# Optimization experiments

Hardware: AMD Instinct MI355X
Metric: run time of the kernel (lower is better)

The kernel has to match this reference:

```python
import jax, jax.numpy as jnp
import numpy as np

B, H, S = 2048, 1024, 128


def setup_inputs() -> dict:
    key = jax.random.key(0)
    ks = jax.random.split(key, 8)
    s = 0.05  # keep gates out of saturation, roughly 1/sqrt(H) init scale
    return {
        "hidden": jax.random.normal(ks[0], (1, B, H), jnp.float32) * s,
        "cell": jax.random.normal(ks[1], (1, B, H), jnp.float32) * s,
        "W_ih": jax.random.normal(ks[2], (4 * H, 1), jnp.float32) * s,
        "W_hh": jax.random.normal(ks[3], (4 * H, H), jnp.float32) * s,
        "b_ih": jax.random.normal(ks[4], (4 * H,), jnp.float32) * s,
        "b_hh": jax.random.normal(ks[5], (4 * H,), jnp.float32) * s,
        "W_fc": jax.random.normal(ks[6], (S, H), jnp.float32) * s,
        "b_fc": jax.random.normal(ks[7], (S,), jnp.float32) * s,
    }


def reference(hidden, cell, W_ih, W_hh, b_ih, b_hh, W_fc, b_fc):
    # prediction from per-step head fc_i fed back as next input.
    h0 = hidden[0]  # [B, H] (num_layers = 1)
    c0 = cell[0]
    b = b_ih + b_hh  # [4H]
    x0 = jnp.zeros((h0.shape[0], 1), h0.dtype)  # initial zero input [B, 1]

    def step(carry, fc_t):
        h, c, x = carry
        Wt, bt = fc_t  # Wt: [H], bt: scalar
        gates = x @ W_ih.T + h @ W_hh.T + b  # [B, 4H], torch gate order i,f,g,o
        i, f, g, o = jnp.split(gates, 4, axis=-1)
        c = jax.nn.sigmoid(f) * c + jax.nn.sigmoid(i) * jnp.tanh(g)
        h = jax.nn.sigmoid(o) * jnp.tanh(c)
        pred = h @ Wt + bt  # [B] (Linear(H,1) then squeeze)
        return (h, c, pred[:, None]), pred

    _, preds = jax.lax.scan(step, (h0, c0, x0), (W_fc, b_fc))  # preds: [S, B]
    return preds.T  # [B, S]
```

## Files before the change

kernel.cpp:

```cpp
#include <hip/hip_runtime.h>
#include <hip/hip_bf16.h>
#include <stdint.h>

#define B_SZ 2048
#define H_SZ 1024
#define S_SZ 128
#define G4   4096
#define BK   64
#define NKK  16
#define BM   128
#define BN   256
#define NJT  16
#define NBLK 256

typedef short short8 __attribute__((ext_vector_type(8)));
typedef int   intx4  __attribute__((ext_vector_type(4)));
typedef float floatx4 __attribute__((ext_vector_type(4)));

#define AS1 __attribute__((address_space(1)))
#define AS3 __attribute__((address_space(3)))

__device__ ushort g_Wp[G4 * H_SZ];
__device__ ushort g_h[2][B_SZ * H_SZ];
__device__ float  g_wih[G4];
__device__ float  g_bias[G4];
__device__ float  g_pp[2][B_SZ][NJT];
__device__ unsigned g_leaf[8 * 32];
__device__ unsigned g_root;
__device__ unsigned g_gen;

__device__ __forceinline__ ushort f2bf(float f) {
  unsigned u = __float_as_uint(f);
  return (ushort)((u + 0x7FFFu + ((u >> 16) & 1u)) >> 16);
}
__device__ __forceinline__ float fsig(float x) { return 1.f / (1.f + __expf(-x)); }
__device__ __forceinline__ float ftanh(float x) { return 1.f - 2.f / (__expf(2.f * x) + 1.f); }

__device__ __forceinline__ void gload16(const void* g, void* l) {
  __builtin_amdgcn_global_load_lds((const AS1 void*)g, (AS3 void*)l, 16, 0, 0);
}

__device__ __forceinline__ void grid_barrier(int grp) {
  __syncthreads();
  if (threadIdx.x == 0) {
    __builtin_amdgcn_fence(__ATOMIC_RELEASE, "agent");
    unsigned gen = __hip_atomic_load(&g_gen, __ATOMIC_RELAXED, __HIP_MEMORY_SCOPE_AGENT);
    unsigned a = __hip_atomic_fetch_add(&g_leaf[grp * 32], 1u, __ATOMIC_RELAXED,
                                        __HIP_MEMORY_SCOPE_AGENT);
    if (a == 31u) {
      __hip_atomic_store(&g_leaf[grp * 32], 0u, __ATOMIC_RELAXED, __HIP_MEMORY_SCOPE_AGENT);
      unsigned r = __hip_atomic_fetch_add(&g_root, 1u, __ATOMIC_RELAXED,
                                          __HIP_MEMORY_SCOPE_AGENT);
      if (r == 7u) {
        __hip_atomic_store(&g_root, 0u, __ATOMIC_RELAXED, __HIP_MEMORY_SCOPE_AGENT);
        __hip_atomic_store(&g_gen, gen + 1u, __ATOMIC_RELAXED, __HIP_MEMORY_SCOPE_AGENT);
      } else {
        while (__hip_atomic_load(&g_gen, __ATOMIC_RELAXED, __HIP_MEMORY_SCOPE_AGENT) == gen)
          __builtin_amdgcn_s_sleep(2);
      }
    } else {
      while (__hip_atomic_load(&g_gen, __ATOMIC_RELAXED, __HIP_MEMORY_SCOPE_AGENT) == gen)
        __builtin_amdgcn_s_sleep(2);
    }
    asm volatile("" ::: "memory");
  }
  __syncthreads();
}


__global__ __launch_bounds__(256) void prep_wpack(const float* __restrict__ Whh) {
  const int gid = blockIdx.x * 256 + threadIdx.x;
  const int j   = gid >> 7;
  const int k8  = (gid & 127) << 3;
  const int gate = (j >> 4) & 3;
  const int h    = ((j >> 6) << 4) | (j & 15);
  const float* src = Whh + (size_t)(gate * H_SZ + h) * H_SZ + k8;
  floatx4 a = *(const floatx4*)src;
  floatx4 b = *(const floatx4*)(src + 4);
  short8 o;
#pragma unroll
  for (int i = 0; i < 4; ++i) o[i] = (short)f2bf(a[i]);
#pragma unroll
  for (int i = 0; i < 4; ++i) o[4 + i] = (short)f2bf(b[i]);
  const size_t dst = (size_t)(j >> 8) * 262144 + (size_t)(k8 >> 6) * 16384 +
                     (size_t)((k8 >> 3) & 7) * 2048 + (size_t)(j & 255) * 8;
  *(short8*)&g_Wp[dst] = o;
}

__global__ __launch_bounds__(256) void prep_misc(const float* __restrict__ Wih,
                                                 const float* __restrict__ bih,
                                                 const float* __restrict__ bhh) {
  if (blockIdx.x == 0) {
    if (threadIdx.x == 0) { g_root = 0u; g_gen = 0u; }
    if (threadIdx.x < 8) g_leaf[threadIdx.x * 32] = 0u;
  }
  const int j = blockIdx.x * 256 + threadIdx.x;
  const int gate = (j >> 4) & 3;
  const int h    = ((j >> 6) << 4) | (j & 15);
  const int jp   = gate * H_SZ + h;
  g_wih[j]  = Wih[jp];
  g_bias[j] = bih[jp] + bhh[jp];
}

__global__ __launch_bounds__(256) void prep_h(const float* __restrict__ hidden) {
  const int gid = blockIdx.x * 256 + threadIdx.x;
  const int o8  = gid << 3;
  short8 o;
#pragma unroll
  for (int i = 0; i < 8; ++i) o[i] = (short)f2bf(hidden[o8 + i]);
  *(short8*)&g_h[0][o8] = o;
}

__global__ __launch_bounds__(512, 1)
void lstm_persistent(const float* __restrict__ cell,
                     const float* __restrict__ Wfc,
                     const float* __restrict__ bfc,
                     float* __restrict__ out) {
  __shared__ ushort Al[2][8256];
  __shared__ ushort Bl[3][16384];
  __shared__ float  xbuf[BM];
  __shared__ float  predp[4 * BM];

  const int tid  = threadIdx.x;
  const int lane = tid & 63;
  const int wid  = tid >> 6;
  const int bid  = blockIdx.x;
  const int grp  = bid & 7;
  const int idx  = bid >> 3;
  const int jt   = (grp << 1) | (idx & 1);
  const int bt   = idx >> 1;
  const int brow = bt * BM;
  const int wr = wid >> 2, wc = wid & 3;
  const int lr = lane & 15, lk = lane >> 4;

  const size_t wbase = (size_t)jt * 262144;
  const size_t abase = (size_t)(brow + (tid >> 2)) * H_SZ + (size_t)(tid & 3) * 16;
  ushort* const awp = &Al[0][((tid & 3) * 2) * 1032 + (tid >> 2) * 8];

  const int hcol = ((jt << 2) + wc) * 16 + lr;
  float wih[4], bb[4];
#pragma unroll
  for (int n = 0; n < 4; ++n) {
    const int col = jt * BN + wc * 64 + n * 16 + lr;
    wih[n] = g_wih[col];
    bb[n]  = g_bias[col];
  }

  float creg[4][4];
#pragma unroll
  for (int m = 0; m < 4; ++m)
#pragma unroll
    for (int r = 0; r < 4; ++r) {
      const int row_l = wr * 64 + m * 16 + lk * 4 + r;
      creg[m][r] = cell[(size_t)(brow + row_l) * H_SZ + hcol];
    }

  intx4 a0, a1, a2, a3;

#define ISSUE_B(I)                                                          \
  {                                                                         \
    const ushort* bs = g_Wp + wbase + (size_t)(I) * 16384 + (size_t)tid * 8;\
    ushort* bd = &Bl[(I) % 3][(tid & 448) * 8];                             \
    gload16(bs, bd);                                                        \
    gload16(bs + 4096, bd + 4096);                                          \
    gload16(bs + 8192, bd + 8192);                                          \
    gload16(bs + 12288, bd + 12288);                                        \
  }

#define ISSUE_A(I, AW0, AW1)                                                \
  {                                                                         \
    const ushort* as_ = hin + abase + (size_t)(I) * 64;                     \
    asm volatile("global_load_dwordx4 %0, %1, off sc0 sc1"                  \
                 : "=v"(AW0) : "v"(as_));                                   \
    asm volatile("global_load_dwordx4 %0, %1, off sc0 sc1"                  \
                 : "=v"(AW1) : "v"(as_ + 8));                               \
  }

#define COMPUTE(BA, BB)                                                     \
  {                                                                         \
    _Pragma("unroll") for (int k2 = 0; k2 < 2; ++k2) {                      \
      const int co = k2 * 4 + lk;                                           \
      short8 a[4], b[4];                                                    \
      _Pragma("unroll") for (int m = 0; m < 4; ++m)                         \
          a[m] = *(const short8*)&Al[BA][co * 1032 + (wr * 64 + m * 16 + lr) * 8]; \
      _Pragma("unroll") for (int n = 0; n < 4; ++n)                         \
          b[n] = *(const short8*)&Bl[BB][co * 2048 + (wc * 64 + n * 16 + lr) * 8]; \
      __builtin_amdgcn_s_setprio(1);                                        \
      _Pragma("unroll") for (int m = 0; m < 4; ++m)                         \
          _Pragma("unroll") for (int n = 0; n < 4; ++n)                     \
              acc[m][n] = __builtin_amdgcn_mfma_f32_16x16x32_bf16(          \
                  a[m], b[n], acc[m][n], 0, 0, 0);                          \
      __builtin_amdgcn_s_setprio(0);                                        \
    }                                                                       \
  }

#define PH(I, AW0, AW1, AR0, AR1)                                           \
  {                                                                         \
    ISSUE_B((I) + 1);                                                       \
    ISSUE_A((I) + 1, AW0, AW1);                                             \
    asm volatile("s_waitcnt vmcnt(6)" ::: "memory");                        \
    __builtin_amdgcn_sched_barrier(0);                                      \
    *(intx4*)(awp + ((I) & 1) * 8256) = AR0;                                \
    *(intx4*)(awp + ((I) & 1) * 8256 + 1032) = AR1;                         \
    asm volatile("s_waitcnt lgkmcnt(0)" ::: "memory");                      \
    __builtin_amdgcn_s_barrier();                                           \
    __builtin_amdgcn_sched_barrier(0);                                      \
    COMPUTE((I) & 1, (I) % 3);                                              \
  }

#define PHLAST                                                              \
  {                                                                         \
    asm volatile("s_waitcnt vmcnt(0)" ::: "memory");                        \
    __builtin_amdgcn_sched_barrier(0);                                      \
    *(intx4*)(awp + 8256) = a2;                                             \
    *(intx4*)(awp + 8256 + 1032) = a3;                                      \
    asm volatile("s_waitcnt lgkmcnt(0)" ::: "memory");                      \
    __builtin_amdgcn_s_barrier();                                           \
    __builtin_amdgcn_sched_barrier(0);                                      \
    COMPUTE(1, 0);                                                          \
  }

  for (int t = 0; t < S_SZ; ++t) {
    const int p = t & 1;
    const ushort* __restrict__ hin = g_h[p];
    ushort* __restrict__ hout      = g_h[p ^ 1];

    floatx4 acc[4][4];
#pragma unroll
    for (int m = 0; m < 4; ++m)
#pragma unroll
      for (int n = 0; n < 4; ++n) acc[m][n] = {0.f, 0.f, 0.f, 0.f};

    ISSUE_B(0);
    ISSUE_A(0, a0, a1);

    PH(0,  a2, a3, a0, a1);
    PH(1,  a0, a1, a2, a3);
    PH(2,  a2, a3, a0, a1);
    PH(3,  a0, a1, a2, a3);
    PH(4,  a2, a3, a0, a1);
    PH(5,  a0, a1, a2, a3);
    PH(6,  a2, a3, a0, a1);
    PH(7,  a0, a1, a2, a3);
    PH(8,  a2, a3, a0, a1);
    PH(9,  a0, a1, a2, a3);
    PH(10, a2, a3, a0, a1);
    PH(11, a0, a1, a2, a3);
    PH(12, a2, a3, a0, a1);
    PH(13, a0, a1, a2, a3);
    PH(14, a2, a3, a0, a1);
    PHLAST;

    if (t > 0 && tid < BM) {
      float s = bfc[t - 1];
      const float* pr = &g_pp[(t - 1) & 1][brow + tid][0];
#pragma unroll
      for (int j = 0; j < NJT; ++j)
        s += __hip_atomic_load(pr + j, __ATOMIC_RELAXED, __HIP_MEMORY_SCOPE_AGENT);
      xbuf[tid] = s;
      if (jt == 0) out[(size_t)(brow + tid) * S_SZ + (t - 1)] = s;
    }
    __syncthreads();

    const float wfc_l = Wfc[(size_t)t * H_SZ + hcol];

#pragma unroll
    for (int m = 0; m < 4; ++m) {
#pragma unroll
      for (int r = 0; r < 4; ++r) {
        const int row_l = wr * 64 + m * 16 + lk * 4 + r;
        const float xv = (t > 0) ? xbuf[row_l] : 0.f;
        float gi = acc[m][0][r] + xv * wih[0] + bb[0];
        float gf = acc[m][1][r] + xv * wih[1] + bb[1];
        float gg = acc[m][2][r] + xv * wih[2] + bb[2];
        float go = acc[m][3][r] + xv * wih[3] + bb[3];
        float cn = fsig(gf) * creg[m][r] + fsig(gi) * ftanh(gg);
        creg[m][r] = cn;
        float hv = fsig(go) * ftanh(cn);
        hout[(size_t)(brow + row_l) * H_SZ + hcol] = f2bf(hv);
        float pp = hv * wfc_l;
        pp += __shfl_xor(pp, 1);
        pp += __shfl_xor(pp, 2);
        pp += __shfl_xor(pp, 4);
        pp += __shfl_xor(pp, 8);
        if (lr == 0) predp[wc * BM + row_l] = pp;
      }
    }
    __syncthreads();
    if (tid < BM)
      g_pp[p][brow + tid][jt] = predp[tid] + predp[BM + tid] +
                                predp[2 * BM + tid] + predp[3 * BM + tid];

    grid_barrier(grp);
  }

  if (jt == 0 && tid < BM) {
    float s = bfc[S_SZ - 1];
    const float* pr = &g_pp[1][brow + tid][0];
#pragma unroll
    for (int j = 0; j < NJT; ++j)
      s += __hip_atomic_load(pr + j, __ATOMIC_RELAXED, __HIP_MEMORY_SCOPE_AGENT);
    out[(size_t)(brow + tid) * S_SZ + (S_SZ - 1)] = s;
  }
#undef ISSUE_B
#undef ISSUE_A
#undef COMPUTE
#undef PH
#undef PHLAST
}

extern "C" void kernel_launch(void* const* d_in, const int* in_sizes, int n_in,
                              void* d_out, int out_size, void* d_ws, size_t ws_size,
                              hipStream_t stream) {
  const float* hidden = (const float*)d_in[0];
  const float* cell   = (const float*)d_in[1];
  const float* W_ih   = (const float*)d_in[2];
  const float* W_hh   = (const float*)d_in[3];
  const float* b_ih   = (const float*)d_in[4];
  const float* b_hh   = (const float*)d_in[5];
  const float* W_fc   = (const float*)d_in[6];
  const float* b_fc   = (const float*)d_in[7];
  float* out = (float*)d_out;

  prep_wpack<<<2048, 256, 0, stream>>>(W_hh);
  prep_misc<<<16, 256, 0, stream>>>(W_ih, b_ih, b_hh);
  prep_h<<<1024, 256, 0, stream>>>(hidden);

  lstm_persistent<<<NBLK, 512, 0, stream>>>(cell, W_fc, b_fc, out);
}
```

Baseline: 5.737 ms.

## Retile persistent LSTM GEMM to 64-row blocks with weights loaded straight into registers

Each block now covers 64 batch rows and 512 gate columns (one grp slice) instead of 128x256. Each wave loads its W_hh fragments directly from global memory into registers with double-buffered register sets, which drops the LDS staging for B. Only the h tile goes through LDS, now with an XOR-swizzled layout and a deeper prefetch of five in flight. The packed weight layout becomes plain row-major, and the cross-block prediction reduction drops from 16 partials to 8. The trade-off is more global or L2 traffic for weights per block and higher register pressure in exchange for less LDS use and fewer barriers.

After: 7.388 ms. 1.29x slower.

```diff
diff --git a/kernel.cpp b/kernel.cpp
--- a/kernel.cpp
+++ b/kernel.cpp
@@ -8,9 +8,8 @@
 #define G4   4096
 #define BK   64
 #define NKK  16
-#define BM   128
-#define BN   256
-#define NJT  16
+#define BM   64
+#define NXP  8
 #define NBLK 256
 
 typedef short short8 __attribute__((ext_vector_type(8)));
@@ -24,7 +23,7 @@
 __device__ ushort g_h[2][B_SZ * H_SZ];
 __device__ float  g_wih[G4];
 __device__ float  g_bias[G4];
-__device__ float  g_pp[2][B_SZ][NJT];
+__device__ float  g_pp[2][B_SZ][NXP];
 __device__ unsigned g_leaf[8 * 32];
 __device__ unsigned g_root;
 __device__ unsigned g_gen;
@@ -35,10 +34,7 @@
 }
 __device__ __forceinline__ float fsig(float x) { return 1.f / (1.f + __expf(-x)); }
 __device__ __forceinline__ float ftanh(float x) { return 1.f - 2.f / (__expf(2.f * x) + 1.f); }
-
-__device__ __forceinline__ void gload16(const void* g, void* l) {
-  __builtin_amdgcn_global_load_lds((const AS1 void*)g, (AS3 void*)l, 16, 0, 0);
-}
+__device__ __forceinline__ short8 as_s8(intx4 v) { return __builtin_bit_cast(short8, v); }
 
 __device__ __forceinline__ void grid_barrier(int grp) {
   __syncthreads();
@@ -82,9 +78,7 @@
   for (int i = 0; i < 4; ++i) o[i] = (short)f2bf(a[i]);
 #pragma unroll
   for (int i = 0; i < 4; ++i) o[4 + i] = (short)f2bf(b[i]);
-  const size_t dst = (size_t)(j >> 8) * 262144 + (size_t)(k8 >> 6) * 16384 +
-                     (size_t)((k8 >> 3) & 7) * 2048 + (size_t)(j & 255) * 8;
-  *(short8*)&g_Wp[dst] = o;
+  *(short8*)&g_Wp[(size_t)j * H_SZ + k8] = o;
 }
 
 __global__ __launch_bounds__(256) void prep_misc(const float* __restrict__ Wih,
@@ -116,32 +110,34 @@
                      const float* __restrict__ Wfc,
                      const float* __restrict__ bfc,
                      float* __restrict__ out) {
-  __shared__ ushort Al[2][8256];
-  __shared__ ushort Bl[3][16384];
+  __shared__ ushort Al[2][BM * BK];
   __shared__ float  xbuf[BM];
-  __shared__ float  predp[4 * BM];
+  __shared__ float  predp[8 * BM];
 
   const int tid  = threadIdx.x;
   const int lane = tid & 63;
   const int wid  = tid >> 6;
   const int bid  = blockIdx.x;
   const int grp  = bid & 7;
-  const int idx  = bid >> 3;
-  const int jt   = (grp << 1) | (idx & 1);
-  const int bt   = idx >> 1;
-  const int brow = bt * BM;
-  const int wr = wid >> 2, wc = wid & 3;
+  const int brow = (bid >> 3) * BM;
   const int lr = lane & 15, lk = lane >> 4;
 
-  const size_t wbase = (size_t)jt * 262144;
-  const size_t abase = (size_t)(brow + (tid >> 2)) * H_SZ + (size_t)(tid & 3) * 16;
-  ushort* const awp = &Al[0][((tid & 3) * 2) * 1032 + (tid >> 2) * 8];
-
-  const int hcol = ((jt << 2) + wc) * 16 + lr;
+  const int row0 = tid >> 3, col0 = tid & 7;
+  const size_t abase = (size_t)(brow + row0) * H_SZ + (size_t)col0 * 8;
+  const int awoff = row0 * BK + ((col0 ^ (row0 & 7)) << 3);
+  ushort* const awA = &Al[0][awoff];
+  ushort* const awB = &Al[1][awoff];
+
+  const int ar0 = (0 * 16 + lr) * BK, ar1 = (1 * 16 + lr) * BK;
+  const int ar2 = (2 * 16 + lr) * BK, ar3 = (3 * 16 + lr) * BK;
+  const int cx0 = (lk * 8) ^ ((lr & 7) << 3);
+  const int cx1 = (32 + lk * 8) ^ ((lr & 7) << 3);
+
+  const int hcol = grp * 128 + wid * 16 + lr;
   float wih[4], bb[4];
 #pragma unroll
   for (int n = 0; n < 4; ++n) {
-    const int col = jt * BN + wc * 64 + n * 16 + lr;
+    const int col = grp * 512 + wid * 64 + n * 16 + lr;
     wih[n] = g_wih[col];
     bb[n]  = g_bias[col];
   }
@@ -151,75 +147,59 @@
   for (int m = 0; m < 4; ++m)
 #pragma unroll
     for (int r = 0; r < 4; ++r) {
-      const int row_l = wr * 64 + m * 16 + lk * 4 + r;
+      const int row_l = m * 16 + lk * 4 + r;
       creg[m][r] = cell[(size_t)(brow + row_l) * H_SZ + hcol];
     }
 
-  intx4 a0, a1, a2, a3;
-
-#define ISSUE_B(I)                                                          \
-  {                                                                         \
-    const ushort* bs = g_Wp + wbase + (size_t)(I) * 16384 + (size_t)tid * 8;\
-    ushort* bd = &Bl[(I) % 3][(tid & 448) * 8];                             \
-    gload16(bs, bd);                                                        \
-    gload16(bs + 4096, bd + 4096);                                          \
-    gload16(bs + 8192, bd + 8192);                                          \
-    gload16(bs + 12288, bd + 12288);                                        \
-  }
-
-#define ISSUE_A(I, AW0, AW1)                                                \
-  {                                                                         \
-    const ushort* as_ = hin + abase + (size_t)(I) * 64;                     \
+#define LB(D, P, O)                                                         \
+  asm volatile("global_load_dwordx4 %0, %1, off offset:" #O                 \
+               : "=v"(D) : "v"(P));
+#define ISSUE_A(R, KK)                                                      \
+  { const ushort* ap_ = hin + abase + (KK) * BK;                            \
     asm volatile("global_load_dwordx4 %0, %1, off sc0 sc1"                  \
-                 : "=v"(AW0) : "v"(as_));                                   \
-    asm volatile("global_load_dwordx4 %0, %1, off sc0 sc1"                  \
-                 : "=v"(AW1) : "v"(as_ + 8));                               \
-  }
-
-#define COMPUTE(BA, BB)                                                     \
-  {                                                                         \
-    _Pragma("unroll") for (int k2 = 0; k2 < 2; ++k2) {                      \
-      const int co = k2 * 4 + lk;                                           \
-      short8 a[4], b[4];                                                    \
-      _Pragma("unroll") for (int m = 0; m < 4; ++m)                         \
-          a[m] = *(const short8*)&Al[BA][co * 1032 + (wr * 64 + m * 16 + lr) * 8]; \
-      _Pragma("unroll") for (int n = 0; n < 4; ++n)                         \
-          b[n] = *(const short8*)&Bl[BB][co * 2048 + (wc * 64 + n * 16 + lr) * 8]; \
-      __builtin_amdgcn_s_setprio(1);                                        \
-      _Pragma("unroll") for (int m = 0; m < 4; ++m)                         \
-          _Pragma("unroll") for (int n = 0; n < 4; ++n)                     \
-              acc[m][n] = __builtin_amdgcn_mfma_f32_16x16x32_bf16(          \
-                  a[m], b[n], acc[m][n], 0, 0, 0);                          \
-      __builtin_amdgcn_s_setprio(0);                                        \
-    }                                                                       \
-  }
-
-#define PH(I, AW0, AW1, AR0, AR1)                                           \
-  {                                                                         \
-    ISSUE_B((I) + 1);                                                       \
-    ISSUE_A((I) + 1, AW0, AW1);                                             \
-    asm volatile("s_waitcnt vmcnt(6)" ::: "memory");                        \
+                 : "=v"(R) : "v"(ap_)); }
+#define ISSUE_B_0                                                           \
+  { LB(b000, wb0, 0) LB(b001, wb0, 64) LB(b010, wb1, 0) LB(b011, wb1, 64)  \
+    LB(b020, wb2, 0) LB(b021, wb2, 64) LB(b030, wb3, 0) LB(b031, wb3, 64)  \
+    wb0 += 64; wb1 += 64; wb2 += 64; wb3 += 64; }
+#define ISSUE_B_1                                                           \
+  { LB(b100, wb0, 0) LB(b101, wb0, 64) LB(b110, wb1, 0) LB(b111, wb1, 64)  \
+    LB(b120, wb2, 0) LB(b121, wb2, 64) LB(b130, wb3, 0) LB(b131, wb3, 64)  \
+    wb0 += 64; wb1 += 64; wb2 += 64; wb3 += 64; }
+
+#define MF(A, B, M, N) acc[M][N] = __builtin_amdgcn_mfma_f32_16x16x32_bf16( \
+    A, as_s8(B), acc[M][N], 0, 0, 0)
+#define CHALF(AB, CX, B0, B1, B2, B3)                                       \
+  { short8 a0 = *(const short8*)&Al[AB][ar0 + CX];                          \
+    short8 a1 = *(const short8*)&Al[AB][ar1 + CX];                          \
+    short8 a2 = *(const short8*)&Al[AB][ar2 + CX];                          \
+    short8 a3 = *(const short8*)&Al[AB][ar3 + CX];                          \
+    __builtin_amdgcn_s_setprio(1);                                          \
+    MF(a0, B0, 0, 0); MF(a0, B1, 0, 1); MF(a0, B2, 0, 2); MF(a0, B3, 0, 3); \
+    MF(a1, B0, 1, 0); MF(a1, B1, 1, 1); MF(a1, B2, 1, 2); MF(a1, B3, 1, 3); \
+    MF(a2, B0, 2, 0); MF(a2, B1, 2, 1); MF(a2, B2, 2, 2); MF(a2, B3, 2, 3); \
+    MF(a3, B0, 3, 0); MF(a3, B1, 3, 1); MF(a3, B2, 3, 2); MF(a3, B3, 3, 3); \
+    __builtin_amdgcn_s_setprio(0); }
+#define COMPUTE_0                                                           \
+  { CHALF(0, cx0, b000, b010, b020, b030)                                   \
+    CHALF(0, cx1, b001, b011, b021, b031) }
+#define COMPUTE_1                                                           \
+  { CHALF(1, cx0, b100, b110, b120, b130)                                   \
+    CHALF(1, cx1, b101, b111, b121, b131) }
+
+#define PH(VN, BI, AI, AW, RS, CM)                                          \
+  { BI AI                                                                   \
+    asm volatile("s_waitcnt vmcnt(" #VN ")" ::: "memory");                  \
     __builtin_amdgcn_sched_barrier(0);                                      \
-    *(intx4*)(awp + ((I) & 1) * 8256) = AR0;                                \
-    *(intx4*)(awp + ((I) & 1) * 8256 + 1032) = AR1;                         \
+    *(intx4*)(AW) = RS;                                                     \
     asm volatile("s_waitcnt lgkmcnt(0)" ::: "memory");                      \
+    __builtin_amdgcn_sched_barrier(0);                                      \
     __builtin_amdgcn_s_barrier();                                           \
     __builtin_amdgcn_sched_barrier(0);                                      \
-    COMPUTE((I) & 1, (I) % 3);                                              \
-  }
-
-#define PHLAST                                                              \
-  {                                                                         \
-    asm volatile("s_waitcnt vmcnt(0)" ::: "memory");                        \
-    __builtin_amdgcn_sched_barrier(0);                                      \
-    *(intx4*)(awp + 8256) = a2;                                             \
-    *(intx4*)(awp + 8256 + 1032) = a3;                                      \
-    asm volatile("s_waitcnt lgkmcnt(0)" ::: "memory");                      \
-    __builtin_amdgcn_s_barrier();                                           \
-    __builtin_amdgcn_sched_barrier(0);                                      \
-    COMPUTE(1, 0);                                                          \
-  }
-
+    CM }
+#define NOP_
+
+#pragma unroll 1
   for (int t = 0; t < S_SZ; ++t) {
     const int p = t & 1;
     const ushort* __restrict__ hin = g_h[p];
@@ -231,34 +211,42 @@
 #pragma unroll
       for (int n = 0; n < 4; ++n) acc[m][n] = {0.f, 0.f, 0.f, 0.f};
 
-    ISSUE_B(0);
-    ISSUE_A(0, a0, a1);
-
-    PH(0,  a2, a3, a0, a1);
-    PH(1,  a0, a1, a2, a3);
-    PH(2,  a2, a3, a0, a1);
-    PH(3,  a0, a1, a2, a3);
-    PH(4,  a2, a3, a0, a1);
-    PH(5,  a0, a1, a2, a3);
-    PH(6,  a2, a3, a0, a1);
-    PH(7,  a0, a1, a2, a3);
-    PH(8,  a2, a3, a0, a1);
-    PH(9,  a0, a1, a2, a3);
-    PH(10, a2, a3, a0, a1);
-    PH(11, a0, a1, a2, a3);
-    PH(12, a2, a3, a0, a1);
-    PH(13, a0, a1, a2, a3);
-    PH(14, a2, a3, a0, a1);
-    PHLAST;
+    intx4 r0, r1, r2, r3, r4;
+    intx4 b000, b001, b010, b011, b020, b021, b030, b031;
+    intx4 b100, b101, b110, b111, b120, b121, b130, b131;
+    const ushort* wb0 = g_Wp + (size_t)(grp * 512 + wid * 64 + 0 * 16 + lr) * H_SZ + lk * 8;
+    const ushort* wb1 = g_Wp + (size_t)(grp * 512 + wid * 64 + 1 * 16 + lr) * H_SZ + lk * 8;
+    const ushort* wb2 = g_Wp + (size_t)(grp * 512 + wid * 64 + 2 * 16 + lr) * H_SZ + lk * 8;
+    const ushort* wb3 = g_Wp + (size_t)(grp * 512 + wid * 64 + 3 * 16 + lr) * H_SZ + lk * 8;
+
+    ISSUE_B_0
+    ISSUE_A(r0, 0) ISSUE_A(r1, 1) ISSUE_A(r2, 2) ISSUE_A(r3, 3)
+
+    PH(12, ISSUE_B_1, ISSUE_A(r4, 4),  awA, r0, COMPUTE_0)
+    PH(10, ISSUE_B_0, ISSUE_A(r0, 5),  awB, r1, COMPUTE_1)
+    PH(10, ISSUE_B_1, ISSUE_A(r1, 6),  awA, r2, COMPUTE_0)
+    PH(10, ISSUE_B_0, ISSUE_A(r2, 7),  awB, r3, COMPUTE_1)
+    PH(10, ISSUE_B_1, ISSUE_A(r3, 8),  awA, r4, COMPUTE_0)
+    PH(10, ISSUE_B_0, ISSUE_A(r4, 9),  awB, r0, COMPUTE_1)
+    PH(10, ISSUE_B_1, ISSUE_A(r0, 10), awA, r1, COMPUTE_0)
+    PH(10, ISSUE_B_0, ISSUE_A(r1, 11), awB, r2, COMPUTE_1)
+    PH(10, ISSUE_B_1, ISSUE_A(r2, 12), awA, r3, COMPUTE_0)
+    PH(10, ISSUE_B_0, ISSUE_A(r3, 13), awB, r4, COMPUTE_1)
+    PH(10, ISSUE_B_1, ISSUE_A(r4, 14), awA, r0, COMPUTE_0)
+    PH(10, ISSUE_B_0, ISSUE_A(r0, 15), awB, r1, COMPUTE_1)
+    PH(9,  ISSUE_B_1, NOP_,            awA, r2, COMPUTE_0)
+    PH(8,  ISSUE_B_0, NOP_,            awB, r3, COMPUTE_1)
+    PH(8,  ISSUE_B_1, NOP_,            awA, r4, COMPUTE_0)
+    PH(0,  NOP_,      NOP_,            awB, r0, COMPUTE_1)
 
     if (t > 0 && tid < BM) {
       float s = bfc[t - 1];
       const float* pr = &g_pp[(t - 1) & 1][brow + tid][0];
 #pragma unroll
-      for (int j = 0; j < NJT; ++j)
-        s += __hip_atomic_load(pr + j, __ATOMIC_RELAXED, __HIP_MEMORY_SCOPE_AGENT);
+      for (int g = 0; g < NXP; ++g)
+        s += __hip_atomic_load(pr + g, __ATOMIC_RELAXED, __HIP_MEMORY_SCOPE_AGENT);
       xbuf[tid] = s;
-      if (jt == 0) out[(size_t)(brow + tid) * S_SZ + (t - 1)] = s;
+      if (grp == 0) out[(size_t)(brow + tid) * S_SZ + (t - 1)] = s;
     }
     __syncthreads();
 
@@ -268,7 +256,7 @@
     for (int m = 0; m < 4; ++m) {
 #pragma unroll
       for (int r = 0; r < 4; ++r) {
-        const int row_l = wr * 64 + m * 16 + lk * 4 + r;
+        const int row_l = m * 16 + lk * 4 + r;
         const float xv = (t > 0) ? xbuf[row_l] : 0.f;
         float gi = acc[m][0][r] + xv * wih[0] + bb[0];
         float gf = acc[m][1][r] + xv * wih[1] + bb[1];
@@ -283,30 +271,38 @@
         pp += __shfl_xor(pp, 2);
         pp += __shfl_xor(pp, 4);
         pp += __shfl_xor(pp, 8);
-        if (lr == 0) predp[wc * BM + row_l] = pp;
+        if (lr == 0) predp[wid * BM + row_l] = pp;
       }
     }
     __syncthreads();
-    if (tid < BM)
-      g_pp[p][brow + tid][jt] = predp[tid] + predp[BM + tid] +
-                                predp[2 * BM + tid] + predp[3 * BM + tid];
+    if (tid < BM) {
+      float s = 0.f;
+#pragma unroll
+      for (int w = 0; w < 8; ++w) s += predp[w * BM + tid];
+      g_pp[p][brow + tid][grp] = s;
+    }
 
     grid_barrier(grp);
   }
 
-  if (jt == 0 && tid < BM) {
+  if (grp == 0 && tid < BM) {
     float s = bfc[S_SZ - 1];
     const float* pr = &g_pp[1][brow + tid][0];
 #pragma unroll
-    for (int j = 0; j < NJT; ++j)
-      s += __hip_atomic_load(pr + j, __ATOMIC_RELAXED, __HIP_MEMORY_SCOPE_AGENT);
+    for (int g = 0; g < NXP; ++g)
+      s += __hip_atomic_load(pr + g, __ATOMIC_RELAXED, __HIP_MEMORY_SCOPE_AGENT);
     out[(size_t)(brow + tid) * S_SZ + (S_SZ - 1)] = s;
   }
-#undef ISSUE_B
+#undef LB
 #undef ISSUE_A
-#undef COMPUTE
+#undef ISSUE_B_0
+#undef ISSUE_B_1
+#undef MF
+#undef CHALF
+#undef COMPUTE_0
+#undef COMPUTE_1
 #undef PH
-#undef PHLAST
+#undef NOP_
 }
 
 extern "C" void kernel_launch(void* const* d_in, const int* in_sizes, int n_in,
```
